# Optimization experiments

Hardware: AMD Instinct MI355X
Metric: run time of the kernel (lower is better)

## Reference

```python
import jax, jax.numpy as jnp
import numpy as np

N_NODES = 100000
N_EDGES = 1600000
NUM_FEATURES = 32
EDGE_DIM = 8
GAT_DIM = 16
HEADS = 4
HID = GAT_DIM * HEADS  # 64
OUT_DIM = 2
NUM_GRAPHS = 64
NEG_SLOPE = 0.2


def setup_inputs() -> dict:
    key = jax.random.key(0)
    ks = jax.random.split(key, 24)
    g = lambda k, shp, fan: jax.random.normal(k, shp, jnp.float32) * (1.0 / np.sqrt(fan))
    inp = {
        'x': jax.random.normal(ks[0], (N_NODES, NUM_FEATURES), jnp.float32),
        'edge_index': jax.random.randint(ks[1], (2, N_EDGES), 0, N_NODES, jnp.int64),
        'edge_attr': jax.random.normal(ks[2], (N_EDGES, EDGE_DIM), jnp.float32),
        'batch': jnp.sort(jax.random.randint(ks[3], (N_NODES,), 0, NUM_GRAPHS, jnp.int64)),
        # input GATConv params (PyG: lin bias-free, att_* of shape [H,C], bias [H*C])
        'W0': g(ks[4], (NUM_FEATURES, HID), NUM_FEATURES),
        'att_src0': g(ks[5], (HEADS, GAT_DIM), GAT_DIM),
        'att_dst0': g(ks[6], (HEADS, GAT_DIM), GAT_DIM),
        'We0': g(ks[7], (EDGE_DIM, HID), EDGE_DIM),
        'att_e0': g(ks[8], (HEADS, GAT_DIM), GAT_DIM),
        'b0': jnp.zeros((HID,), jnp.float32),
        # 2 hidden GATConv layers, stacked on a leading layer axis
        'Wh': g(ks[9], (2, HID, HID), HID),
        'att_src_h': g(ks[10], (2, HEADS, GAT_DIM), GAT_DIM),
        'att_dst_h': g(ks[11], (2, HEADS, GAT_DIM), GAT_DIM),
        'We_h': g(ks[12], (2, EDGE_DIM, HID), EDGE_DIM),
        'att_e_h': g(ks[13], (2, HEADS, GAT_DIM), GAT_DIM),
        'bh': jnp.zeros((2, HID), jnp.float32),
        # MLP head
        'fc1_w': g(ks[14], (HID, 2 * GAT_DIM), HID),
        'fc1_b': jnp.zeros((2 * GAT_DIM,), jnp.float32),
        'fc2_w': g(ks[15], (2 * GAT_DIM, OUT_DIM), 2 * GAT_DIM),
        'fc2_b': jnp.zeros((OUT_DIM,), jnp.float32),
    }
    return inp


def _gat_conv(x, src, dst, ea, W, a_s, a_d, We, a_e, b, n_nodes):
    # x: [N, Fin] -> out: [N, H*C]
    xp = (x @ W).reshape(n_nodes, HEADS, GAT_DIM)
    al_s = jnp.einsum('nhc,hc->nh', xp, a_s)            # per-node src logits
    al_d = jnp.einsum('nhc,hc->nh', xp, a_d)
    ep = (ea @ We).reshape(-1, HEADS, GAT_DIM)
    al_e = jnp.einsum('ehc,hc->eh', ep, a_e)
    alpha = jax.nn.leaky_relu(al_s[src] + al_d[dst] + al_e, NEG_SLOPE)  # [E,H]
    m = jax.ops.segment_max(alpha, dst, num_segments=n_nodes)
    m = jnp.where(jnp.isfinite(m), m, 0.0)              # nodes with no in-edges
    ex = jnp.exp(alpha - m[dst])
    den = jax.ops.segment_sum(ex, dst, num_segments=n_nodes)
    coef = ex / (den[dst] + 1e-16)                      # segment softmax over dst
    out = jax.ops.segment_sum(xp[src] * coef[..., None], dst, num_segments=n_nodes)
    return out.reshape(n_nodes, HID) + b


def _forward(x, edge_index, edge_attr, batch, W0, att_src0, att_dst0, We0, att_e0,
             b0, Wh, att_src_h, att_dst_h, We_h, att_e_h, bh, fc1_w, fc1_b, fc2_w, fc2_b):
    n = x.shape[0]
    src, dst = edge_index[0], edge_index[1]
    # PyG add_self_loops(fill_value='mean'): self-loop attr = mean of incoming edge attrs
    cnt = jax.ops.segment_sum(jnp.ones((src.shape[0],), x.dtype), dst, num_segments=n)
    mean_attr = jax.ops.segment_sum(edge_attr, dst, num_segments=n) / jnp.clip(cnt, 1.0)[:, None]
    loop = jnp.arange(n, dtype=src.dtype)
    src_sl = jnp.concatenate([src, loop])
    dst_sl = jnp.concatenate([dst, loop])
    ea_sl = jnp.concatenate([edge_attr, mean_attr], axis=0)

    h = _gat_conv(x, src_sl, dst_sl, ea_sl, W0, att_src0, att_dst0, We0, att_e0, b0, n)
    h = jax.nn.relu(h)
    for i in range(2):  # source has `x - F.relu(x)` (no-op): no ReLU between hidden layers
        h = _gat_conv(h, src_sl, dst_sl, ea_sl, Wh[i], att_src_h[i], att_dst_h[i],
                      We_h[i], att_e_h[i], bh[i], n)
    # global_mean_pool over graphs
    ones = jnp.ones((n,), h.dtype)
    gcnt = jax.ops.segment_sum(ones, batch, num_segments=NUM_GRAPHS)
    pooled = jax.ops.segment_sum(h, batch, num_segments=NUM_GRAPHS) / jnp.clip(gcnt, 1.0)[:, None]
    y = jax.nn.relu(pooled @ fc1_w + fc1_b)
    return y @ fc2_w + fc2_b


def reference(x, edge_index, edge_attr, batch, W0, att_src0, att_dst0, We0, att_e0,
              b0, Wh, att_src_h, att_dst_h, We_h, att_e_h, bh, fc1_w, fc1_b, fc2_w, fc2_b):
    return _forward(x, edge_index, edge_attr, batch, W0, att_src0, att_dst0, We0, att_e0,
                    b0, Wh, att_src_h, att_dst_h, We_h, att_e_h, bh, fc1_w, fc1_b, fc2_w, fc2_b)
```

## Files before the change

### kernel.cpp

```cpp
#include <hip/hip_runtime.h>
#include <hip/hip_bf16.h>
#include <hip/hip_fp16.h>

#define N_NODES 100000
#define N_EDGES 1600000
#define E_SL (N_EDGES + N_NODES)
#define HID 64
#define NUM_GRAPHS 64
#define NEG_SLOPE 0.2f
#define SCAN_CHUNK 1024
#define SCAN_NB ((N_NODES + SCAN_CHUNK - 1) / SCAN_CHUNK)
#define ROW_W 8
#define XP_NODES_PER_BLK 16
#define POOL_NODES_PER_BLK 256


__global__ void hist_kernel(const int* __restrict__ ei, int* __restrict__ cnt,
                            int* __restrict__ rank) {
    int e = blockIdx.x * blockDim.x + threadIdx.x;
    if (e >= N_EDGES) return;
    rank[e] = atomicAdd(&cnt[ei[N_EDGES + e]], 1);
}

__global__ void scan_local_kernel(const int* __restrict__ cnt, int* __restrict__ row_ptr,
                                  int* __restrict__ bsum) {
    __shared__ int s[256];
    int t = threadIdx.x;
    int base = blockIdx.x * SCAN_CHUNK + t * 4;
    int v[4]; int sum = 0;
    #pragma unroll
    for (int i = 0; i < 4; ++i) {
        int idx = base + i;
        v[i] = (idx < N_NODES) ? cnt[idx] + 1 : 0;
        sum += v[i];
    }
    s[t] = sum;
    __syncthreads();
    for (int off = 1; off < 256; off <<= 1) {
        int x = (t >= off) ? s[t - off] : 0;
        __syncthreads();
        s[t] += x;
        __syncthreads();
    }
    int run = s[t] - sum;
    #pragma unroll
    for (int i = 0; i < 4; ++i) {
        int idx = base + i;
        if (idx < N_NODES) row_ptr[idx] = run;
        run += v[i];
    }
    if (t == 255) bsum[blockIdx.x] = s[255];
}

__global__ void scan_bsum_kernel(int* __restrict__ bsum) {
    if (threadIdx.x != 0) return;
    int acc = 0;
    for (int i = 0; i < SCAN_NB; ++i) { int v = bsum[i]; bsum[i] = acc; acc += v; }
}

__global__ void scan_add_kernel(int* __restrict__ row_ptr, const int* __restrict__ bsum) {
    int i = blockIdx.x * blockDim.x + threadIdx.x;
    if (i > N_NODES) return;
    if (i == N_NODES) row_ptr[i] = E_SL;
    else row_ptr[i] += bsum[i >> 10];
}

__global__ void weff_all_kernel(const float* __restrict__ We0, const float* __restrict__ ae0,
                                const float* __restrict__ Weh, const float* __restrict__ aeh,
                                float* __restrict__ weff) {
    int t = threadIdx.x;
    if (t >= 96) return;
    int layer = t >> 5, r = t & 31;
    int dd = r >> 2, h = r & 3;
    const float* We = (layer == 0) ? We0 : Weh + (size_t)(layer - 1) * 8 * 64;
    const float* ae = (layer == 0) ? ae0 : aeh + (size_t)(layer - 1) * 64;
    float s = 0.f;
    #pragma unroll
    for (int c = 0; c < 16; ++c) s += We[dd * 64 + h * 16 + c] * ae[h * 16 + c];
    weff[layer * 32 + dd * 4 + h] = s;
}

__global__ void build_csr_kernel(const int* __restrict__ ei, const float* __restrict__ ea,
                                 const int* __restrict__ row_ptr,
                                 const int* __restrict__ rank,
                                 const float* __restrict__ weff,
                                 unsigned int* __restrict__ ale_csr) {
    int e = blockIdx.x * blockDim.x + threadIdx.x;
    if (e >= N_EDGES) return;
    int src = ei[e];
    int d = ei[N_EDGES + e];
    float4 a0 = *(const float4*)(ea + (size_t)e * 8);
    float4 a1 = *(const float4*)(ea + (size_t)e * 8 + 4);
    float av[8] = {a0.x, a0.y, a0.z, a0.w, a1.x, a1.y, a1.z, a1.w};
    unsigned int w[8];
    #pragma unroll
    for (int l = 0; l < 3; ++l) {
        float al[4];
        #pragma unroll
        for (int h = 0; h < 4; ++h) {
            float s = 0.f;
            #pragma unroll
            for (int j = 0; j < 8; ++j) s += av[j] * weff[l * 32 + j * 4 + h];
            al[h] = s;
        }
        __half2 p01 = __floats2half2_rn(al[0], al[1]);
        __half2 p23 = __floats2half2_rn(al[2], al[3]);
        w[2 * l]     = *(unsigned int*)&p01;
        w[2 * l + 1] = *(unsigned int*)&p23;
    }
    w[6] = (unsigned int)src;
    w[7] = 0u;
    int pos = row_ptr[d] + rank[e];
    unsigned int* rowp = ale_csr + (size_t)pos * ROW_W;
    *(uint4*)rowp       = make_uint4(w[0], w[1], w[2], w[3]);
    *(uint4*)(rowp + 4) = make_uint4(w[4], w[5], w[6], w[7]);
}

__global__ void mean_ea_kernel(const int* __restrict__ row_ptr,
                               unsigned int* __restrict__ ale_csr) {
    int idx = blockIdx.x * blockDim.x + threadIdx.x;
    if (idx >= N_NODES * 2) return;
    int n = idx >> 1, part = idx & 1;
    int start = row_ptr[n], last = row_ptr[n + 1] - 1;
    float inv = 1.f / fmaxf((float)(last - start), 1.f);
    if (part == 0) {
        float s[8] = {0.f, 0.f, 0.f, 0.f, 0.f, 0.f, 0.f, 0.f};
        for (int pos = start; pos < last; ++pos) {
            uint4 v = *(const uint4*)(ale_csr + (size_t)pos * ROW_W);
            float2 f0 = __half22float2(*(const __half2*)&v.x);
            float2 f1 = __half22float2(*(const __half2*)&v.y);
            float2 f2 = __half22float2(*(const __half2*)&v.z);
            float2 f3 = __half22float2(*(const __half2*)&v.w);
            s[0] += f0.x; s[1] += f0.y; s[2] += f1.x; s[3] += f1.y;
            s[4] += f2.x; s[5] += f2.y; s[6] += f3.x; s[7] += f3.y;
        }
        __half2 p0 = __floats2half2_rn(s[0] * inv, s[1] * inv);
        __half2 p1 = __floats2half2_rn(s[2] * inv, s[3] * inv);
        __half2 p2 = __floats2half2_rn(s[4] * inv, s[5] * inv);
        __half2 p3 = __floats2half2_rn(s[6] * inv, s[7] * inv);
        *(uint4*)(ale_csr + (size_t)last * ROW_W) =
            make_uint4(*(unsigned int*)&p0, *(unsigned int*)&p1,
                       *(unsigned int*)&p2, *(unsigned int*)&p3);
    } else {
        float s[4] = {0.f, 0.f, 0.f, 0.f};
        for (int pos = start; pos < last; ++pos) {
            uint2 v = *(const uint2*)(ale_csr + (size_t)pos * ROW_W + 4);
            float2 f0 = __half22float2(*(const __half2*)&v.x);
            float2 f1 = __half22float2(*(const __half2*)&v.y);
            s[0] += f0.x; s[1] += f0.y; s[2] += f1.x; s[3] += f1.y;
        }
        __half2 p0 = __floats2half2_rn(s[0] * inv, s[1] * inv);
        __half2 p1 = __floats2half2_rn(s[2] * inv, s[3] * inv);
        uint4 w = make_uint4(*(unsigned int*)&p0, *(unsigned int*)&p1,
                             (unsigned int)n, 0u);
        *(uint4*)(ale_csr + (size_t)last * ROW_W + 4) = w;
    }
}


template <int FIN>
__global__ __launch_bounds__(64) void xp_kernel(
    const float* __restrict__ xin, const float* __restrict__ W,
    const float* __restrict__ a_s, const float* __restrict__ a_d,
    __half* __restrict__ xp, float* __restrict__ als, float* __restrict__ ald) {
    int lane = threadIdx.x;
    float wcol[FIN];
    #pragma unroll
    for (int k = 0; k < FIN; ++k) wcol[k] = W[k * 64 + lane];
    float asl = a_s[lane], adl = a_d[lane];
    int n0 = blockIdx.x * XP_NODES_PER_BLK;
    #pragma unroll 1
    for (int ni = 0; ni < XP_NODES_PER_BLK; ++ni) {
        int n = n0 + ni;
        if (n >= N_NODES) return;
        const float* xr = xin + (size_t)n * FIN;
        float a0 = 0.f, a1 = 0.f, a2 = 0.f, a3 = 0.f;
        #pragma unroll
        for (int k = 0; k < FIN; k += 4) {
            float4 xv = *(const float4*)(xr + k);
            a0 += xv.x * wcol[k];     a1 += xv.y * wcol[k + 1];
            a2 += xv.z * wcol[k + 2]; a3 += xv.w * wcol[k + 3];
        }
        float acc = (a0 + a1) + (a2 + a3);
        xp[(size_t)n * 64 + lane] = __float2half(acc);
        float ps = acc * asl, pd = acc * adl;
        #pragma unroll
        for (int mk = 8; mk >= 1; mk >>= 1) {
            ps += __shfl_xor(ps, mk, 16);
            pd += __shfl_xor(pd, mk, 16);
        }
        if ((lane & 15) == 0) {
            als[(size_t)n * 4 + (lane >> 4)] = ps;
            ald[(size_t)n * 4 + (lane >> 4)] = pd;
        }
    }
}

__global__ __launch_bounds__(256) void gat_node_kernel(
    const int* __restrict__ row_ptr, const unsigned int* __restrict__ ale_csr,
    const float* __restrict__ als, const float* __restrict__ ald,
    const __half* __restrict__ xp, int layer,
    float* __restrict__ out, const float* __restrict__ bias, int relu_flag) {
    __shared__ float exl[4 * 256];
    __shared__ int   coll[4 * 64];
    int wave = threadIdx.x >> 6, lane = threadIdx.x & 63;
    int node = blockIdx.x * 4 + wave;
    if (node >= N_NODES) return;
    int start = row_ptr[node], end = row_ptr[node + 1];
    int deg = end - start;
    int wb = wave * 64, wb4 = wave * 256;
    int cq = lane & 15;
    int eg = lane >> 4;
    int hv = cq >> 2;

    float4 ad4 = *(const float4*)(ald + (size_t)node * 4);

    float4 acc4 = make_float4(0.f, 0.f, 0.f, 0.f);
    float csum = 0.f;

    for (int base = 0; base < deg; base += 64) {
        int cnt = min(64, deg - base);
        float ex0 = 0.f, ex1 = 0.f, ex2 = 0.f, ex3 = 0.f;
        int s = 0;
        if (lane < cnt) {
            const unsigned int* row = ale_csr + (size_t)(start + base + lane) * ROW_W;
            uint2 alew = *(const uint2*)(row + 2 * layer);
            s = (int)row[6];
            float2 e01 = __half22float2(*(const __half2*)&alew.x);
            float2 e23 = __half22float2(*(const __half2*)&alew.y);
            float4 as4 = *(const float4*)(als + (size_t)s * 4);
            float v0 = as4.x + ad4.x + e01.x;
            float v1 = as4.y + ad4.y + e01.y;
            float v2 = as4.z + ad4.z + e23.x;
            float v3 = as4.w + ad4.w + e23.y;
            ex0 = expf((v0 >= 0.f) ? v0 : NEG_SLOPE * v0);
            ex1 = expf((v1 >= 0.f) ? v1 : NEG_SLOPE * v1);
            ex2 = expf((v2 >= 0.f) ? v2 : NEG_SLOPE * v2);
            ex3 = expf((v3 >= 0.f) ? v3 : NEG_SLOPE * v3);
        }
        *(float4*)(exl + wb4 + lane * 4) = make_float4(ex0, ex1, ex2, ex3);
        coll[wb + lane] = s;
        const float* exw = exl + wb4 + hv;
        int cntUp = (cnt + 15) & ~15;
        for (int j = eg; j < cntUp; j += 16) {
            int s0 = coll[wb + j],     s1 = coll[wb + j + 4];
            int s2 = coll[wb + j + 8], s3 = coll[wb + j + 12];
            float c0 = exw[(j) * 4],      c1 = exw[(j + 4) * 4];
            float c2 = exw[(j + 8) * 4],  c3 = exw[(j + 12) * 4];
            uint2 x0 = *(const uint2*)(xp + (size_t)s0 * 64 + cq * 4);
            uint2 x1 = *(const uint2*)(xp + (size_t)s1 * 64 + cq * 4);
            uint2 x2 = *(const uint2*)(xp + (size_t)s2 * 64 + cq * 4);
            uint2 x3 = *(const uint2*)(xp + (size_t)s3 * 64 + cq * 4);
            float2 f00 = __half22float2(*(const __half2*)&x0.x);
            float2 f01 = __half22float2(*(const __half2*)&x0.y);
            float2 f10 = __half22float2(*(const __half2*)&x1.x);
            float2 f11 = __half22float2(*(const __half2*)&x1.y);
            float2 f20 = __half22float2(*(const __half2*)&x2.x);
            float2 f21 = __half22float2(*(const __half2*)&x2.y);
            float2 f30 = __half22float2(*(const __half2*)&x3.x);
            float2 f31 = __half22float2(*(const __half2*)&x3.y);
            acc4.x += c0 * f00.x + c1 * f10.x + c2 * f20.x + c3 * f30.x;
            acc4.y += c0 * f00.y + c1 * f10.y + c2 * f20.y + c3 * f30.y;
            acc4.z += c0 * f01.x + c1 * f11.x + c2 * f21.x + c3 * f31.x;
            acc4.w += c0 * f01.y + c1 * f11.y + c2 * f21.y + c3 * f31.y;
            csum   += c0 + c1 + c2 + c3;
        }
    }
    #pragma unroll
    for (int mk = 16; mk < 64; mk <<= 1) {
        acc4.x += __shfl_xor(acc4.x, mk);
        acc4.y += __shfl_xor(acc4.y, mk);
        acc4.z += __shfl_xor(acc4.z, mk);
        acc4.w += __shfl_xor(acc4.w, mk);
        csum   += __shfl_xor(csum, mk);
    }
    if (eg == 0) {
        float inv = 1.f / (csum + 1e-16f);
        float4 b4 = *(const float4*)(bias + cq * 4);
        float4 v;
        v.x = acc4.x * inv + b4.x;
        v.y = acc4.y * inv + b4.y;
        v.z = acc4.z * inv + b4.z;
        v.w = acc4.w * inv + b4.w;
        if (relu_flag) {
            v.x = fmaxf(v.x, 0.f); v.y = fmaxf(v.y, 0.f);
            v.z = fmaxf(v.z, 0.f); v.w = fmaxf(v.w, 0.f);
        }
        *(float4*)(out + (size_t)node * 64 + cq * 4) = v;
    }
}

__global__ void pool_kernel(const float* __restrict__ h, const int* __restrict__ batch,
                            float* __restrict__ pooled) {
    int base = blockIdx.x * POOL_NODES_PER_BLK;
    int tid = threadIdx.x;
    int c = tid & 63, r = tid >> 6;
    float acc = 0.f;
    int curg = -1;
    for (int i = r; i < POOL_NODES_PER_BLK; i += 4) {
        int n = base + i;
        if (n >= N_NODES) break;
        int g = batch[n];
        if (g != curg) {
            if (curg >= 0) atomicAdd(&pooled[curg * 64 + c], acc);
            curg = g; acc = 0.f;
        }
        acc += h[(size_t)n * 64 + c];
    }
    if (curg >= 0) atomicAdd(&pooled[curg * 64 + c], acc);
}

__global__ void mlp_kernel(const float* __restrict__ pooled, const int* __restrict__ batch,
                           const float* __restrict__ w1, const float* __restrict__ b1,
                           const float* __restrict__ w2, const float* __restrict__ b2,
                           float* __restrict__ y) {
    int g = blockIdx.x, t = threadIdx.x;
    __shared__ float p[64], f1[32];
    __shared__ float invc_s;
    if (t == 0) {
        int lo = 0, hi = N_NODES;
        while (lo < hi) { int mid = (lo + hi) >> 1; if (batch[mid] < g) lo = mid + 1; else hi = mid; }
        int start = lo;
        hi = N_NODES;
        while (lo < hi) { int mid = (lo + hi) >> 1; if (batch[mid] < g + 1) lo = mid + 1; else hi = mid; }
        invc_s = 1.f / fmaxf((float)(lo - start), 1.f);
    }
    __syncthreads();
    p[t] = pooled[g * 64 + t] * invc_s;
    __syncthreads();
    if (t < 32) {
        float a = b1[t];
        #pragma unroll
        for (int k = 0; k < 64; ++k) a += p[k] * w1[k * 32 + t];
        f1[t] = fmaxf(a, 0.f);
    }
    __syncthreads();
    if (t < 2) {
        float a = b2[t];
        #pragma unroll
        for (int k = 0; k < 32; ++k) a += f1[k] * w2[k * 2 + t];
        y[g * 2 + t] = a;
    }
}

extern "C" void kernel_launch(void* const* d_in, const int* in_sizes, int n_in,
                              void* d_out, int out_size, void* d_ws, size_t ws_size,
                              hipStream_t stream) {
    const float* x    = (const float*)d_in[0];
    const int*   ei   = (const int*)d_in[1];
    const float* ea   = (const float*)d_in[2];
    const int*   batch= (const int*)d_in[3];
    const float* W0   = (const float*)d_in[4];
    const float* as0  = (const float*)d_in[5];
    const float* ad0  = (const float*)d_in[6];
    const float* We0  = (const float*)d_in[7];
    const float* ae0  = (const float*)d_in[8];
    const float* b0   = (const float*)d_in[9];
    const float* Wh   = (const float*)d_in[10];
    const float* ash  = (const float*)d_in[11];
    const float* adh  = (const float*)d_in[12];
    const float* Weh  = (const float*)d_in[13];
    const float* aeh  = (const float*)d_in[14];
    const float* bh   = (const float*)d_in[15];
    const float* w1   = (const float*)d_in[16];
    const float* b1   = (const float*)d_in[17];
    const float* w2   = (const float*)d_in[18];
    const float* b2   = (const float*)d_in[19];
    float* out = (float*)d_out;

    char* wsb = (char*)d_ws;
    size_t off = 0;
    auto alloc = [&](size_t bytes) { char* p = wsb + off; off += (bytes + 255) & ~(size_t)255; return p; };
    int*          row_ptr = (int*)alloc((size_t)(N_NODES + 1) * 4);
    unsigned int* ale_csr = (unsigned int*)alloc((size_t)E_SL * ROW_W * 4);
    float*        als     = (float*)alloc((size_t)N_NODES * 4 * 4);
    float*        ald     = (float*)alloc((size_t)N_NODES * 4 * 4);
    float*        weff    = (float*)alloc(3 * 32 * 4);
    float*        pooled  = (float*)alloc((size_t)NUM_GRAPHS * 64 * 4);
    __half*       bufA    = (__half*)alloc((size_t)N_NODES * 64 * 2);
    float*        bufB    = (float*)alloc((size_t)N_NODES * 64 * 4);
    int* cnt  = (int*)bufB;
    int* bsum = cnt + N_NODES;
    int* rank = bsum + ((SCAN_NB + 63) & ~63);

    weff_all_kernel<<<1, 128, 0, stream>>>(We0, ae0, Weh, aeh, weff);
    hipMemsetAsync(cnt, 0, (size_t)N_NODES * 4, stream);
    hist_kernel<<<(N_EDGES + 255) / 256, 256, 0, stream>>>(ei, cnt, rank);
    scan_local_kernel<<<SCAN_NB, 256, 0, stream>>>(cnt, row_ptr, bsum);
    scan_bsum_kernel<<<1, 64, 0, stream>>>(bsum);
    scan_add_kernel<<<(N_NODES + 256) / 256, 256, 0, stream>>>(row_ptr, bsum);
    build_csr_kernel<<<(N_EDGES + 255) / 256, 256, 0, stream>>>(
        ei, ea, row_ptr, rank, weff, ale_csr);
    mean_ea_kernel<<<(N_NODES * 2 + 255) / 256, 256, 0, stream>>>(row_ptr, ale_csr);

    for (int layer = 0; layer < 3; ++layer) {
        const float *W, *as_, *ad_, *bb, *xin;
        int relu_flag = (layer == 0);
        if (layer == 0) {
            W = W0; as_ = as0; ad_ = ad0; bb = b0; xin = x;
        } else {
            int i = layer - 1;
            W   = Wh  + (size_t)i * 64 * 64;
            as_ = ash + (size_t)i * 64;
            ad_ = adh + (size_t)i * 64;
            bb  = bh  + (size_t)i * 64;
            xin = bufB;
        }
        int xpgrid = (N_NODES + XP_NODES_PER_BLK - 1) / XP_NODES_PER_BLK;
        if (layer == 0)
            xp_kernel<32><<<xpgrid, 64, 0, stream>>>(xin, W, as_, ad_, bufA, als, ald);
        else
            xp_kernel<64><<<xpgrid, 64, 0, stream>>>(xin, W, as_, ad_, bufA, als, ald);
        gat_node_kernel<<<(N_NODES + 3) / 4, 256, 0, stream>>>(
            row_ptr, ale_csr, als, ald, bufA, layer, bufB, bb, relu_flag);
    }
    hipMemsetAsync(pooled, 0, (size_t)NUM_GRAPHS * 64 * 4, stream);
    pool_kernel<<<(N_NODES + POOL_NODES_PER_BLK - 1) / POOL_NODES_PER_BLK, 256, 0, stream>>>(
        bufB, batch, pooled);
    mlp_kernel<<<NUM_GRAPHS, 64, 0, stream>>>(pooled, batch, w1, b1, w2, b2, out);
}
```

Before: 625.4 us.

## Split per-layer edge logits into compact arrays and parallelize mean edge-attr

Adds a transpose kernel that splits the 32-byte CSR edge rows into three per-layer 12-byte rows (two half2 logit words plus source index), so each GAT layer reads only the bytes it uses. This path is enabled only when the workspace is large enough. The mean edge-attribute kernel now uses 8 lanes per node with strided 16-byte loads and a shuffle reduction, replacing two serial threads per node. The cost is an extra pass that reads and writes the full edge array, plus more workspace.

```diff
diff --git a/kernel.cpp b/kernel.cpp
--- a/kernel.cpp
+++ b/kernel.cpp
@@ -11,6 +11,7 @@
 #define SCAN_CHUNK 1024
 #define SCAN_NB ((N_NODES + SCAN_CHUNK - 1) / SCAN_CHUNK)
 #define ROW_W 8
+#define TROW_W 3
 #define XP_NODES_PER_BLK 16
 #define POOL_NODES_PER_BLK 256
 
@@ -118,22 +119,28 @@
 
 __global__ void mean_ea_kernel(const int* __restrict__ row_ptr,
                                unsigned int* __restrict__ ale_csr) {
-    int idx = blockIdx.x * blockDim.x + threadIdx.x;
-    if (idx >= N_NODES * 2) return;
-    int n = idx >> 1, part = idx & 1;
+    int t = blockIdx.x * blockDim.x + threadIdx.x;
+    int n = t >> 3;
+    if (n >= N_NODES) return;
+    int j = t & 7;
     int start = row_ptr[n], last = row_ptr[n + 1] - 1;
+    float s[8] = {0.f, 0.f, 0.f, 0.f, 0.f, 0.f, 0.f, 0.f};
+    for (int idx = start * 2 + j; idx < last * 2; idx += 8) {
+        uint4 v = *(const uint4*)(ale_csr + (size_t)idx * 4);
+        float2 f0 = __half22float2(*(const __half2*)&v.x);
+        float2 f1 = __half22float2(*(const __half2*)&v.y);
+        float2 f2 = __half22float2(*(const __half2*)&v.z);
+        float2 f3 = __half22float2(*(const __half2*)&v.w);
+        s[0] += f0.x; s[1] += f0.y; s[2] += f1.x; s[3] += f1.y;
+        s[4] += f2.x; s[5] += f2.y; s[6] += f3.x; s[7] += f3.y;
+    }
+    #pragma unroll
+    for (int mk = 2; mk <= 4; mk <<= 1) {
+        #pragma unroll
+        for (int q = 0; q < 8; ++q) s[q] += __shfl_xor(s[q], mk);
+    }
     float inv = 1.f / fmaxf((float)(last - start), 1.f);
-    if (part == 0) {
-        float s[8] = {0.f, 0.f, 0.f, 0.f, 0.f, 0.f, 0.f, 0.f};
-        for (int pos = start; pos < last; ++pos) {
-            uint4 v = *(const uint4*)(ale_csr + (size_t)pos * ROW_W);
-            float2 f0 = __half22float2(*(const __half2*)&v.x);
-            float2 f1 = __half22float2(*(const __half2*)&v.y);
-            float2 f2 = __half22float2(*(const __half2*)&v.z);
-            float2 f3 = __half22float2(*(const __half2*)&v.w);
-            s[0] += f0.x; s[1] += f0.y; s[2] += f1.x; s[3] += f1.y;
-            s[4] += f2.x; s[5] += f2.y; s[6] += f3.x; s[7] += f3.y;
-        }
+    if (j == 0) {
         __half2 p0 = __floats2half2_rn(s[0] * inv, s[1] * inv);
         __half2 p1 = __floats2half2_rn(s[2] * inv, s[3] * inv);
         __half2 p2 = __floats2half2_rn(s[4] * inv, s[5] * inv);
@@ -141,20 +148,29 @@
         *(uint4*)(ale_csr + (size_t)last * ROW_W) =
             make_uint4(*(unsigned int*)&p0, *(unsigned int*)&p1,
                        *(unsigned int*)&p2, *(unsigned int*)&p3);
-    } else {
-        float s[4] = {0.f, 0.f, 0.f, 0.f};
-        for (int pos = start; pos < last; ++pos) {
-            uint2 v = *(const uint2*)(ale_csr + (size_t)pos * ROW_W + 4);
-            float2 f0 = __half22float2(*(const __half2*)&v.x);
-            float2 f1 = __half22float2(*(const __half2*)&v.y);
-            s[0] += f0.x; s[1] += f0.y; s[2] += f1.x; s[3] += f1.y;
-        }
+    } else if (j == 1) {
         __half2 p0 = __floats2half2_rn(s[0] * inv, s[1] * inv);
         __half2 p1 = __floats2half2_rn(s[2] * inv, s[3] * inv);
-        uint4 w = make_uint4(*(unsigned int*)&p0, *(unsigned int*)&p1,
-                             (unsigned int)n, 0u);
-        *(uint4*)(ale_csr + (size_t)last * ROW_W + 4) = w;
-    }
+        *(uint4*)(ale_csr + (size_t)last * ROW_W + 4) =
+            make_uint4(*(unsigned int*)&p0, *(unsigned int*)&p1,
+                       (unsigned int)n, 0u);
+    }
+}
+
+__global__ void transpose_ale_kernel(const unsigned int* __restrict__ ale_csr,
+                                     unsigned int* __restrict__ ale_t) {
+    int pos = blockIdx.x * blockDim.x + threadIdx.x;
+    if (pos >= E_SL) return;
+    const unsigned int* row = ale_csr + (size_t)pos * ROW_W;
+    uint4 w0 = *(const uint4*)row;
+    uint4 w1 = *(const uint4*)(row + 4);
+    unsigned int src = w1.z;
+    unsigned int* t0 = ale_t + (size_t)pos * TROW_W;
+    t0[0] = w0.x; t0[1] = w0.y; t0[2] = src;
+    unsigned int* t1 = ale_t + ((size_t)E_SL + pos) * TROW_W;
+    t1[0] = w0.z; t1[1] = w0.w; t1[2] = src;
+    unsigned int* t2 = ale_t + ((size_t)2 * E_SL + pos) * TROW_W;
+    t2[0] = w1.x; t2[1] = w1.y; t2[2] = src;
 }
 
 
@@ -196,8 +212,9 @@
     }
 }
 
+template <bool TRANSPOSED>
 __global__ __launch_bounds__(256) void gat_node_kernel(
-    const int* __restrict__ row_ptr, const unsigned int* __restrict__ ale_csr,
+    const int* __restrict__ row_ptr, const unsigned int* __restrict__ aleB,
     const float* __restrict__ als, const float* __restrict__ ald,
     const __half* __restrict__ xp, int layer,
     float* __restrict__ out, const float* __restrict__ bias, int relu_flag) {
@@ -223,11 +240,18 @@
         float ex0 = 0.f, ex1 = 0.f, ex2 = 0.f, ex3 = 0.f;
         int s = 0;
         if (lane < cnt) {
-            const unsigned int* row = ale_csr + (size_t)(start + base + lane) * ROW_W;
-            uint2 alew = *(const uint2*)(row + 2 * layer);
-            s = (int)row[6];
-            float2 e01 = __half22float2(*(const __half2*)&alew.x);
-            float2 e23 = __half22float2(*(const __half2*)&alew.y);
+            int pos = start + base + lane;
+            unsigned int wa, wb_;
+            if (TRANSPOSED) {
+                const unsigned int* row = aleB + (size_t)pos * TROW_W;
+                wa = row[0]; wb_ = row[1]; s = (int)row[2];
+            } else {
+                const unsigned int* row = aleB + (size_t)pos * ROW_W;
+                uint2 alew = *(const uint2*)(row + 2 * layer);
+                wa = alew.x; wb_ = alew.y; s = (int)row[6];
+            }
+            float2 e01 = __half22float2(*(const __half2*)&wa);
+            float2 e23 = __half22float2(*(const __half2*)&wb_);
             float4 as4 = *(const float4*)(als + (size_t)s * 4);
             float v0 = as4.x + ad4.x + e01.x;
             float v1 = as4.y + ad4.y + e01.y;
@@ -368,11 +392,15 @@
     const float* b2   = (const float*)d_in[19];
     float* out = (float*)d_out;
 
+    const int use_t = (ws_size >= (size_t)160 * 1000 * 1000) ? 1 : 0;
+
     char* wsb = (char*)d_ws;
     size_t off = 0;
     auto alloc = [&](size_t bytes) { char* p = wsb + off; off += (bytes + 255) & ~(size_t)255; return p; };
     int*          row_ptr = (int*)alloc((size_t)(N_NODES + 1) * 4);
     unsigned int* ale_csr = (unsigned int*)alloc((size_t)E_SL * ROW_W * 4);
+    unsigned int* ale_t   = use_t ? (unsigned int*)alloc((size_t)E_SL * TROW_W * 4 * 3)
+                                  : (unsigned int*)nullptr;
     float*        als     = (float*)alloc((size_t)N_NODES * 4 * 4);
     float*        ald     = (float*)alloc((size_t)N_NODES * 4 * 4);
     float*        weff    = (float*)alloc(3 * 32 * 4);
@@ -391,7 +419,9 @@
     scan_add_kernel<<<(N_NODES + 256) / 256, 256, 0, stream>>>(row_ptr, bsum);
     build_csr_kernel<<<(N_EDGES + 255) / 256, 256, 0, stream>>>(
         ei, ea, row_ptr, rank, weff, ale_csr);
-    mean_ea_kernel<<<(N_NODES * 2 + 255) / 256, 256, 0, stream>>>(row_ptr, ale_csr);
+    mean_ea_kernel<<<(N_NODES * 8 + 255) / 256, 256, 0, stream>>>(row_ptr, ale_csr);
+    if (use_t)
+        transpose_ale_kernel<<<(E_SL + 255) / 256, 256, 0, stream>>>(ale_csr, ale_t);
 
     for (int layer = 0; layer < 3; ++layer) {
         const float *W, *as_, *ad_, *bb, *xin;
@@ -411,8 +441,13 @@
             xp_kernel<32><<<xpgrid, 64, 0, stream>>>(xin, W, as_, ad_, bufA, als, ald);
         else
             xp_kernel<64><<<xpgrid, 64, 0, stream>>>(xin, W, as_, ad_, bufA, als, ald);
-        gat_node_kernel<<<(N_NODES + 3) / 4, 256, 0, stream>>>(
-            row_ptr, ale_csr, als, ald, bufA, layer, bufB, bb, relu_flag);
+        if (use_t)
+            gat_node_kernel<true><<<(N_NODES + 3) / 4, 256, 0, stream>>>(
+                row_ptr, ale_t + (size_t)layer * E_SL * TROW_W, als, ald, bufA, layer,
+                bufB, bb, relu_flag);
+        else
+            gat_node_kernel<false><<<(N_NODES + 3) / 4, 256, 0, stream>>>(
+                row_ptr, ale_csr, als, ald, bufA, layer, bufB, bb, relu_flag);
     }
     hipMemsetAsync(pooled, 0, (size_t)NUM_GRAPHS * 64 * 4, stream);
     pool_kernel<<<(N_NODES + POOL_NODES_PER_BLK - 1) / POOL_NODES_PER_BLK, 256, 0, stream>>>(
```

Result: no change. 628.3 us (+0.5%).
